# Performance work log

Measured on AMD Instinct MI355X. Metric: run time of the kernel, lower is better.

The kernel has to match this reference:

```python
import jax, jax.numpy as jnp
import numpy as np

GROUP_SIZE = 128
LORA_ALPHA = 32
R = 16
SCALING = LORA_ALPHA / R  # lora_alpha / r


def setup_inputs() -> dict:
    key = jax.random.key(0)
    k1, k2, k3, k4, k5, k6 = jax.random.split(key, 6)
    B, S, IN, OUT = 8, 16, 4096, 11008
    G = IN // GROUP_SIZE  # 32 quantization groups
    x = jax.random.normal(k1, (B, S, IN), dtype=jnp.float32)
    int_weight = jax.random.randint(k2, (IN, OUT), 0, 16, dtype=jnp.int32)  # int4 codes
    zeros = jax.random.randint(k3, (G, OUT), 0, 16, dtype=jnp.int32)        # per-group zero points
    scales = jax.random.uniform(k4, (G, OUT), dtype=jnp.float32) * 0.02     # per-group scales
    lora_A = jax.random.normal(k5, (R, IN), dtype=jnp.float32) * (1.0 / np.sqrt(IN))
    lora_B = jax.random.normal(k6, (OUT, R), dtype=jnp.float32) * 0.02
    return {"x": x, "int_weight": int_weight, "zeros": zeros,
            "scales": scales, "lora_A": lora_A, "lora_B": lora_B}


def reference(x, int_weight, zeros, scales, lora_A, lora_B):
    # Dequantize int4 weights: w[i, o] = (q[i, o] - zero[g(i), o]) * scale[g(i), o]
    zeros_f = jnp.repeat(zeros.astype(jnp.float32), GROUP_SIZE, axis=0)   # [IN, OUT]
    scales_f = jnp.repeat(scales, GROUP_SIZE, axis=0)                     # [IN, OUT]
    w = (int_weight.astype(jnp.float32) - zeros_f) * scales_f             # [IN, OUT]
    # qlinear: x @ W_deq
    base = jnp.einsum('bsi,io->bso', x, w)
    # LoRA: x @ A^T @ B^T * scaling  (dropout=0 -> identity)
    lora = jnp.einsum('bsr,or->bso', jnp.einsum('bsi,ri->bsr', x, lora_A), lora_B)
    return base + lora * SCALING
```

## Files before the change

### kernel.cpp

```cpp
#include <hip/hip_runtime.h>
#include <hip/hip_bf16.h>

typedef __bf16 bf16_t;
typedef __bf16 bf16x8 __attribute__((ext_vector_type(8)));
typedef __bf16 bf16x4 __attribute__((ext_vector_type(4)));
typedef float f32x4 __attribute__((ext_vector_type(4)));

#define M_TOK 128
#define K_IN 4096
#define N_OUT 11008
#define R_LORA 16
#define SCALING 2.0f

__global__ __launch_bounds__(256) void k_prep(const float* __restrict__ x,
                                              const float* __restrict__ loraA,
                                              float* __restrict__ T,
                                              bf16_t* __restrict__ xb) {
  const int m = blockIdx.x;
  __shared__ float xs[K_IN];
  const float4* xr = (const float4*)(x + (size_t)m * K_IN);
  bf16x4* xbr = (bf16x4*)(xb + (size_t)m * K_IN);
  for (int i = threadIdx.x; i < K_IN / 4; i += 256) {
    float4 v = xr[i];
    ((float4*)xs)[i] = v;
    bf16x4 pv = {(bf16_t)v.x, (bf16_t)v.y, (bf16_t)v.z, (bf16_t)v.w};
    xbr[i] = pv;
  }
  __syncthreads();
  const int w = threadIdx.x >> 6;
  const int lane = threadIdx.x & 63;
  float a0 = 0.f, a1 = 0.f, a2 = 0.f, a3 = 0.f;
  const float4* A0 = (const float4*)(loraA + (size_t)(w * 4 + 0) * K_IN);
  const float4* A1 = (const float4*)(loraA + (size_t)(w * 4 + 1) * K_IN);
  const float4* A2 = (const float4*)(loraA + (size_t)(w * 4 + 2) * K_IN);
  const float4* A3 = (const float4*)(loraA + (size_t)(w * 4 + 3) * K_IN);
  for (int i = lane; i < K_IN / 4; i += 64) {
    float4 xv = ((float4*)xs)[i];
    float4 v0 = A0[i], v1 = A1[i], v2 = A2[i], v3 = A3[i];
    a0 += xv.x * v0.x + xv.y * v0.y + xv.z * v0.z + xv.w * v0.w;
    a1 += xv.x * v1.x + xv.y * v1.y + xv.z * v1.z + xv.w * v1.w;
    a2 += xv.x * v2.x + xv.y * v2.y + xv.z * v2.z + xv.w * v2.w;
    a3 += xv.x * v3.x + xv.y * v3.y + xv.z * v3.z + xv.w * v3.w;
  }
#pragma unroll
  for (int off = 32; off; off >>= 1) {
    a0 += __shfl_down(a0, off);
    a1 += __shfl_down(a1, off);
    a2 += __shfl_down(a2, off);
    a3 += __shfl_down(a3, off);
  }
  if (lane == 0) {
    float* tm = T + m * R_LORA + w * 4;
    tm[0] = a0 * SCALING;
    tm[1] = a1 * SCALING;
    tm[2] = a2 * SCALING;
    tm[3] = a3 * SCALING;
  }
}

__global__ __launch_bounds__(256) void k_lora(const float* __restrict__ T,
                                              const float* __restrict__ loraB,
                                              float* __restrict__ out) {
  const int b = blockIdx.x;
  const int m = b / 43;
  const int o = (b % 43) * 256 + threadIdx.x;
  const float* t = T + m * R_LORA;
  const float4* br = (const float4*)(loraB + (size_t)o * R_LORA);
  float4 b0 = br[0], b1 = br[1], b2 = br[2], b3 = br[3];
  float s = t[0] * b0.x + t[1] * b0.y + t[2] * b0.z + t[3] * b0.w +
            t[4] * b1.x + t[5] * b1.y + t[6] * b1.z + t[7] * b1.w +
            t[8] * b2.x + t[9] * b2.y + t[10] * b2.z + t[11] * b2.w +
            t[12] * b3.x + t[13] * b3.y + t[14] * b3.z + t[15] * b3.w;
  out[(size_t)m * N_OUT + o] = s;
}

#define NSTRIPS 172
#define WSTRIDE 72

__global__ __launch_bounds__(256, 4) void k_main(const int* __restrict__ qw,
                                                 const int* __restrict__ zr,
                                                 const float* __restrict__ sc,
                                                 const bf16_t* __restrict__ xb,
                                                 float* __restrict__ out) {
  const int nb = blockIdx.x % NSTRIPS;
  const int kc = blockIdx.x / NSTRIPS;
  const int o0 = nb * 64;
  const int k0 = kc * 1024;

  __shared__ __align__(16) bf16_t wlds[2][64 * WSTRIDE];

  const int tid = threadIdx.x;
  const int w = tid >> 6;
  const int lane = tid & 63;
  const int oq = lane;
  const int kq = w * 16;
  const int ocol = o0 + oq;
  const int* qp = qw + (size_t)(k0 + kq) * N_OUT + ocol;

  float sf[8], nzs[8];
  {
    const int g0 = k0 >> 7;
#pragma unroll
    for (int g = 0; g < 8; ++g) {
      float s_ = sc[(size_t)(g0 + g) * N_OUT + ocol];
      int z_ = zr[(size_t)(g0 + g) * N_OUT + ocol];
      sf[g] = s_;
      nzs[g] = -(float)z_ * s_;
    }
  }

  int qr[16];
#pragma unroll
  for (int j = 0; j < 16; ++j) qr[j] = qp[(size_t)j * N_OUT];
  {
    bf16x8 wv0, wv1;
#pragma unroll
    for (int j = 0; j < 8; ++j) {
      wv0[j] = (bf16_t)fmaf((float)qr[j], sf[0], nzs[0]);
      wv1[j] = (bf16_t)fmaf((float)qr[8 + j], sf[0], nzs[0]);
    }
    *(bf16x8*)&wlds[0][oq * WSTRIDE + kq] = wv0;
    *(bf16x8*)&wlds[0][oq * WSTRIDE + kq + 8] = wv1;
  }

  f32x4 acc[2][4];
#pragma unroll
  for (int mt = 0; mt < 2; ++mt)
#pragma unroll
    for (int ot = 0; ot < 4; ++ot) acc[mt][ot] = (f32x4){0.f, 0.f, 0.f, 0.f};

  const int aq = (lane >> 4) * 8;
  const bf16_t* ap = xb + (size_t)(w * 32 + (lane & 15)) * K_IN + k0 + aq;

#pragma unroll
  for (int step = 0; step < 16; ++step) {
    __syncthreads();
    const int buf = step & 1;

    if (step + 1 < 16) {
      const int* qn = qp + (size_t)(step + 1) * 64 * N_OUT;
#pragma unroll
      for (int j = 0; j < 16; ++j) qr[j] = qn[(size_t)j * N_OUT];
    }

#pragma unroll
    for (int ks = 0; ks < 2; ++ks) {
      bf16x8 a0 = *(const bf16x8*)(ap + step * 64 + ks * 32);
      bf16x8 a1 = *(const bf16x8*)(ap + (size_t)16 * K_IN + step * 64 + ks * 32);
#pragma unroll
      for (int ot = 0; ot < 4; ++ot) {
        bf16x8 bfrag =
            *(bf16x8*)&wlds[buf][(ot * 16 + (lane & 15)) * WSTRIDE + ks * 32 + aq];
        acc[0][ot] = __builtin_amdgcn_mfma_f32_16x16x32_bf16(a0, bfrag, acc[0][ot], 0, 0, 0);
        acc[1][ot] = __builtin_amdgcn_mfma_f32_16x16x32_bf16(a1, bfrag, acc[1][ot], 0, 0, 0);
      }
    }

    if (step + 1 < 16) {
      const int g = (step + 1) >> 1;
      bf16x8 wv0, wv1;
#pragma unroll
      for (int j = 0; j < 8; ++j) {
        wv0[j] = (bf16_t)fmaf((float)qr[j], sf[g], nzs[g]);
        wv1[j] = (bf16_t)fmaf((float)qr[8 + j], sf[g], nzs[g]);
      }
      *(bf16x8*)&wlds[1 - buf][oq * WSTRIDE + kq] = wv0;
      *(bf16x8*)&wlds[1 - buf][oq * WSTRIDE + kq + 8] = wv1;
    }
  }

#pragma unroll
  for (int mt = 0; mt < 2; ++mt) {
    const int m = w * 32 + mt * 16 + ((lane >> 4) << 2);
#pragma unroll
    for (int ot = 0; ot < 4; ++ot) {
      const int o = o0 + ot * 16 + (lane & 15);
#pragma unroll
      for (int r = 0; r < 4; ++r)
        unsafeAtomicAdd(&out[(size_t)(m + r) * N_OUT + o], acc[mt][ot][r]);
    }
  }
}

extern "C" void kernel_launch(void* const* d_in, const int* in_sizes, int n_in,
                              void* d_out, int out_size, void* d_ws, size_t ws_size,
                              hipStream_t stream) {
  const float* x = (const float*)d_in[0];
  const int* qw = (const int*)d_in[1];
  const int* zr = (const int*)d_in[2];
  const float* sc = (const float*)d_in[3];
  const float* loraA = (const float*)d_in[4];
  const float* loraB = (const float*)d_in[5];
  float* out = (float*)d_out;

  float* T = (float*)d_ws;
  bf16_t* xb = (bf16_t*)((char*)d_ws + 8192);

  k_prep<<<dim3(M_TOK), dim3(256), 0, stream>>>(x, loraA, T, xb);
  k_lora<<<dim3(M_TOK * 43), dim3(256), 0, stream>>>(T, loraB, out);
  k_main<<<dim3(NSTRIPS * 4), dim3(256), 0, stream>>>(qw, zr, sc, xb, out);
}
```

Baseline: 292.7 us.

## Restructure main GEMM into 16-column tiles with in-block split-K reduction and fused LoRA epilogue

The main kernel now gives each block a 16-wide output strip covering all 128 tokens. Its four waves each take a quarter of K, dequantize weights straight into registers as MFMA B fragments with no LDS staging, and reduce through shared memory. The LoRA B projection is fused into the epilogue, so the separate k_lora kernel and the global atomics go away and outputs are written with plain vector stores. The prep kernel writes x in an MFMA-fragment-friendly bf16 layout so A loads are coalesced. The cost is that A fragments are re-read from global/L2 by every block, and occupancy hint drops to 3.

```diff
diff --git a/kernel.cpp b/kernel.cpp
--- a/kernel.cpp
+++ b/kernel.cpp
@@ -3,7 +3,6 @@
 
 typedef __bf16 bf16_t;
 typedef __bf16 bf16x8 __attribute__((ext_vector_type(8)));
-typedef __bf16 bf16x4 __attribute__((ext_vector_type(4)));
 typedef float f32x4 __attribute__((ext_vector_type(4)));
 
 #define M_TOK 128
@@ -11,20 +10,28 @@
 #define N_OUT 11008
 #define R_LORA 16
 #define SCALING 2.0f
+#define NTILE 688
 
 __global__ __launch_bounds__(256) void k_prep(const float* __restrict__ x,
                                               const float* __restrict__ loraA,
                                               float* __restrict__ T,
-                                              bf16_t* __restrict__ xb) {
+                                              bf16_t* __restrict__ xf) {
   const int m = blockIdx.x;
+  const int mt = m >> 4;
+  const int ml = m & 15;
   __shared__ float xs[K_IN];
   const float4* xr = (const float4*)(x + (size_t)m * K_IN);
-  bf16x4* xbr = (bf16x4*)(xb + (size_t)m * K_IN);
-  for (int i = threadIdx.x; i < K_IN / 4; i += 256) {
-    float4 v = xr[i];
-    ((float4*)xs)[i] = v;
-    bf16x4 pv = {(bf16_t)v.x, (bf16_t)v.y, (bf16_t)v.z, (bf16_t)v.w};
-    xbr[i] = pv;
+#pragma unroll
+  for (int c0 = 0; c0 < 2; ++c0) {
+    const int c = c0 * 256 + threadIdx.x;
+    float4 vA = xr[2 * c], vB = xr[2 * c + 1];
+    ((float4*)xs)[2 * c] = vA;
+    ((float4*)xs)[2 * c + 1] = vB;
+    bf16x8 pv = {(bf16_t)vA.x, (bf16_t)vA.y, (bf16_t)vA.z, (bf16_t)vA.w,
+                 (bf16_t)vB.x, (bf16_t)vB.y, (bf16_t)vB.z, (bf16_t)vB.w};
+    const int ks = c >> 2;
+    const int lq = (c & 3) * 16 + ml;
+    *(bf16x8*)(xf + ((size_t)(mt * 128 + ks) * 64 + lq) * 8) = pv;
   }
   __syncthreads();
   const int w = threadIdx.x >> 6;
@@ -58,44 +65,27 @@
   }
 }
 
-__global__ __launch_bounds__(256) void k_lora(const float* __restrict__ T,
-                                              const float* __restrict__ loraB,
-                                              float* __restrict__ out) {
-  const int b = blockIdx.x;
-  const int m = b / 43;
-  const int o = (b % 43) * 256 + threadIdx.x;
-  const float* t = T + m * R_LORA;
-  const float4* br = (const float4*)(loraB + (size_t)o * R_LORA);
-  float4 b0 = br[0], b1 = br[1], b2 = br[2], b3 = br[3];
-  float s = t[0] * b0.x + t[1] * b0.y + t[2] * b0.z + t[3] * b0.w +
-            t[4] * b1.x + t[5] * b1.y + t[6] * b1.z + t[7] * b1.w +
-            t[8] * b2.x + t[9] * b2.y + t[10] * b2.z + t[11] * b2.w +
-            t[12] * b3.x + t[13] * b3.y + t[14] * b3.z + t[15] * b3.w;
-  out[(size_t)m * N_OUT + o] = s;
-}
-
-#define NSTRIPS 172
-#define WSTRIDE 72
-
-__global__ __launch_bounds__(256, 4) void k_main(const int* __restrict__ qw,
+__global__ __launch_bounds__(256, 3) void k_main(const int* __restrict__ qw,
                                                  const int* __restrict__ zr,
                                                  const float* __restrict__ sc,
-                                                 const bf16_t* __restrict__ xb,
+                                                 const bf16_t* __restrict__ xf,
+                                                 const float* __restrict__ T,
+                                                 const float* __restrict__ loraB,
                                                  float* __restrict__ out) {
-  const int nb = blockIdx.x % NSTRIPS;
-  const int kc = blockIdx.x / NSTRIPS;
-  const int o0 = nb * 64;
-  const int k0 = kc * 1024;
-
-  __shared__ __align__(16) bf16_t wlds[2][64 * WSTRIDE];
-
+  const int nt = (blockIdx.x & 7) * 86 + (blockIdx.x >> 3);
+  const int o0 = nt * 16;
   const int tid = threadIdx.x;
   const int w = tid >> 6;
   const int lane = tid & 63;
-  const int oq = lane;
-  const int kq = w * 16;
-  const int ocol = o0 + oq;
-  const int* qp = qw + (size_t)(k0 + kq) * N_OUT + ocol;
+  const int ol = lane & 15;
+  const int ocol = o0 + ol;
+  const int krow = (lane >> 4) * 8;
+  const int k0 = w * 1024;
+
+  __shared__ float red[4][M_TOK * 16];
+  __shared__ float lb[256];
+
+  lb[tid] = loraB[(size_t)o0 * R_LORA + tid];
 
   float sf[8], nzs[8];
   {
@@ -109,77 +99,88 @@
     }
   }
 
-  int qr[16];
-#pragma unroll
-  for (int j = 0; j < 16; ++j) qr[j] = qp[(size_t)j * N_OUT];
+  const int* qp = qw + (size_t)(k0 + krow) * N_OUT + ocol;
+  const bf16_t* ap = xf + ((size_t)(k0 >> 5) * 64 + lane) * 8;
+
+  int qA[8], qB[8];
+#pragma unroll
+  for (int j = 0; j < 8; ++j) qA[j] = qp[(size_t)j * N_OUT];
   {
-    bf16x8 wv0, wv1;
-#pragma unroll
-    for (int j = 0; j < 8; ++j) {
-      wv0[j] = (bf16_t)fmaf((float)qr[j], sf[0], nzs[0]);
-      wv1[j] = (bf16_t)fmaf((float)qr[8 + j], sf[0], nzs[0]);
-    }
-    *(bf16x8*)&wlds[0][oq * WSTRIDE + kq] = wv0;
-    *(bf16x8*)&wlds[0][oq * WSTRIDE + kq + 8] = wv1;
-  }
-
-  f32x4 acc[2][4];
-#pragma unroll
-  for (int mt = 0; mt < 2; ++mt)
-#pragma unroll
-    for (int ot = 0; ot < 4; ++ot) acc[mt][ot] = (f32x4){0.f, 0.f, 0.f, 0.f};
-
-  const int aq = (lane >> 4) * 8;
-  const bf16_t* ap = xb + (size_t)(w * 32 + (lane & 15)) * K_IN + k0 + aq;
-
-#pragma unroll
-  for (int step = 0; step < 16; ++step) {
-    __syncthreads();
-    const int buf = step & 1;
-
-    if (step + 1 < 16) {
-      const int* qn = qp + (size_t)(step + 1) * 64 * N_OUT;
-#pragma unroll
-      for (int j = 0; j < 16; ++j) qr[j] = qn[(size_t)j * N_OUT];
-    }
-
-#pragma unroll
-    for (int ks = 0; ks < 2; ++ks) {
-      bf16x8 a0 = *(const bf16x8*)(ap + step * 64 + ks * 32);
-      bf16x8 a1 = *(const bf16x8*)(ap + (size_t)16 * K_IN + step * 64 + ks * 32);
-#pragma unroll
-      for (int ot = 0; ot < 4; ++ot) {
-        bf16x8 bfrag =
-            *(bf16x8*)&wlds[buf][(ot * 16 + (lane & 15)) * WSTRIDE + ks * 32 + aq];
-        acc[0][ot] = __builtin_amdgcn_mfma_f32_16x16x32_bf16(a0, bfrag, acc[0][ot], 0, 0, 0);
-        acc[1][ot] = __builtin_amdgcn_mfma_f32_16x16x32_bf16(a1, bfrag, acc[1][ot], 0, 0, 0);
-      }
-    }
-
-    if (step + 1 < 16) {
-      const int g = (step + 1) >> 1;
-      bf16x8 wv0, wv1;
-#pragma unroll
-      for (int j = 0; j < 8; ++j) {
-        wv0[j] = (bf16_t)fmaf((float)qr[j], sf[g], nzs[g]);
-        wv1[j] = (bf16_t)fmaf((float)qr[8 + j], sf[g], nzs[g]);
-      }
-      *(bf16x8*)&wlds[1 - buf][oq * WSTRIDE + kq] = wv0;
-      *(bf16x8*)&wlds[1 - buf][oq * WSTRIDE + kq + 8] = wv1;
-    }
-  }
-
-#pragma unroll
-  for (int mt = 0; mt < 2; ++mt) {
-    const int m = w * 32 + mt * 16 + ((lane >> 4) << 2);
-#pragma unroll
-    for (int ot = 0; ot < 4; ++ot) {
-      const int o = o0 + ot * 16 + (lane & 15);
-#pragma unroll
-      for (int r = 0; r < 4; ++r)
-        unsafeAtomicAdd(&out[(size_t)(m + r) * N_OUT + o], acc[mt][ot][r]);
-    }
-  }
+    const int* qn = qp + (size_t)32 * N_OUT;
+#pragma unroll
+    for (int j = 0; j < 8; ++j) qB[j] = qn[(size_t)j * N_OUT];
+  }
+
+  f32x4 acc[8];
+#pragma unroll
+  for (int mt = 0; mt < 8; ++mt) acc[mt] = (f32x4){0.f, 0.f, 0.f, 0.f};
+
+  for (int kk = 0; kk < 32; kk += 2) {
+    const int g = kk >> 2;
+    bf16x8 bfA;
+#pragma unroll
+    for (int j = 0; j < 8; ++j) bfA[j] = (bf16_t)fmaf((float)qA[j], sf[g], nzs[g]);
+    if (kk < 30) {
+      const int* qn = qp + (size_t)(kk + 2) * 32 * N_OUT;
+#pragma unroll
+      for (int j = 0; j < 8; ++j) qA[j] = qn[(size_t)j * N_OUT];
+    }
+#pragma unroll
+    for (int mt = 0; mt < 8; ++mt) {
+      bf16x8 a = *(const bf16x8*)(ap + ((size_t)mt * 128 + kk) * 512);
+      acc[mt] = __builtin_amdgcn_mfma_f32_16x16x32_bf16(a, bfA, acc[mt], 0, 0, 0);
+    }
+    bf16x8 bfB;
+#pragma unroll
+    for (int j = 0; j < 8; ++j) bfB[j] = (bf16_t)fmaf((float)qB[j], sf[g], nzs[g]);
+    if (kk < 30) {
+      const int* qn = qp + (size_t)(kk + 3) * 32 * N_OUT;
+#pragma unroll
+      for (int j = 0; j < 8; ++j) qB[j] = qn[(size_t)j * N_OUT];
+    }
+#pragma unroll
+    for (int mt = 0; mt < 8; ++mt) {
+      bf16x8 a = *(const bf16x8*)(ap + ((size_t)mt * 128 + kk + 1) * 512);
+      acc[mt] = __builtin_amdgcn_mfma_f32_16x16x32_bf16(a, bfB, acc[mt], 0, 0, 0);
+    }
+  }
+
+#pragma unroll
+  for (int mt = 0; mt < 8; ++mt) {
+    const int mbase = mt * 16 + ((lane >> 4) << 2);
+#pragma unroll
+    for (int r = 0; r < 4; ++r) red[w][(mbase + r) * 16 + ol] = acc[mt][r];
+  }
+  __syncthreads();
+
+  const int m = tid >> 1;
+  const int ob = (tid & 1) * 8;
+  float tr[16];
+  {
+    const float4* Tm4 = (const float4*)(T + (size_t)m * R_LORA);
+#pragma unroll
+    for (int q = 0; q < 4; ++q) {
+      float4 tv = Tm4[q];
+      tr[q * 4 + 0] = tv.x;
+      tr[q * 4 + 1] = tv.y;
+      tr[q * 4 + 2] = tv.z;
+      tr[q * 4 + 3] = tv.w;
+    }
+  }
+  float res[8];
+#pragma unroll
+  for (int i = 0; i < 8; ++i) {
+    const int e = m * 16 + ob + i;
+    float s = red[0][e] + red[1][e] + red[2][e] + red[3][e];
+    const float* lr = &lb[(ob + i) * R_LORA];
+    float tv = 0.f;
+#pragma unroll
+    for (int r = 0; r < 16; ++r) tv = fmaf(tr[r], lr[r], tv);
+    res[i] = s + tv;
+  }
+  float4* op = (float4*)(out + (size_t)m * N_OUT + o0 + ob);
+  op[0] = (float4){res[0], res[1], res[2], res[3]};
+  op[1] = (float4){res[4], res[5], res[6], res[7]};
 }
 
 extern "C" void kernel_launch(void* const* d_in, const int* in_sizes, int n_in,
@@ -194,9 +195,8 @@
   float* out = (float*)d_out;
 
   float* T = (float*)d_ws;
-  bf16_t* xb = (bf16_t*)((char*)d_ws + 8192);
-
-  k_prep<<<dim3(M_TOK), dim3(256), 0, stream>>>(x, loraA, T, xb);
-  k_lora<<<dim3(M_TOK * 43), dim3(256), 0, stream>>>(T, loraB, out);
-  k_main<<<dim3(NSTRIPS * 4), dim3(256), 0, stream>>>(qw, zr, sc, xb, out);
+  bf16_t* xf = (bf16_t*)((char*)d_ws + 8192);
+
+  k_prep<<<dim3(M_TOK), dim3(256), 0, stream>>>(x, loraA, T, xf);
+  k_main<<<dim3(NTILE), dim3(256), 0, stream>>>(qw, zr, sc, xf, T, loraB, out);
 }
```

New measurement: 319.8 us. 9.2% more time.

## Deepen weight prefetch to two stages and pre-swizzle bf16 activations into MFMA fragments

Applied to the files above, without the earlier changes.

The main loop now keeps two register sets of int4 codes in flight, issuing global loads two steps ahead instead of one, so more latency of the weight stream is hidden behind the MFMAs. The prep kernel also writes x in a fragment-major layout so each lane's A-operand load is one contiguous 16-byte read with lanes adjacent, rather than strided row accesses. The cost is 16 more live registers per thread, which may pressure the 4-blocks-per-SIMD occupancy target.

```diff
diff --git a/kernel.cpp b/kernel.cpp
--- a/kernel.cpp
+++ b/kernel.cpp
@@ -3,7 +3,6 @@
 
 typedef __bf16 bf16_t;
 typedef __bf16 bf16x8 __attribute__((ext_vector_type(8)));
-typedef __bf16 bf16x4 __attribute__((ext_vector_type(4)));
 typedef float f32x4 __attribute__((ext_vector_type(4)));
 
 #define M_TOK 128
@@ -11,20 +10,29 @@
 #define N_OUT 11008
 #define R_LORA 16
 #define SCALING 2.0f
+#define NSTRIPS 172
+#define WSTRIDE 72
 
 __global__ __launch_bounds__(256) void k_prep(const float* __restrict__ x,
                                               const float* __restrict__ loraA,
                                               float* __restrict__ T,
-                                              bf16_t* __restrict__ xb) {
+                                              bf16_t* __restrict__ xf) {
   const int m = blockIdx.x;
+  const int mt = m >> 4;
+  const int ml = m & 15;
   __shared__ float xs[K_IN];
   const float4* xr = (const float4*)(x + (size_t)m * K_IN);
-  bf16x4* xbr = (bf16x4*)(xb + (size_t)m * K_IN);
-  for (int i = threadIdx.x; i < K_IN / 4; i += 256) {
-    float4 v = xr[i];
-    ((float4*)xs)[i] = v;
-    bf16x4 pv = {(bf16_t)v.x, (bf16_t)v.y, (bf16_t)v.z, (bf16_t)v.w};
-    xbr[i] = pv;
+#pragma unroll
+  for (int c0 = 0; c0 < 2; ++c0) {
+    const int c = c0 * 256 + threadIdx.x;
+    float4 vA = xr[2 * c], vB = xr[2 * c + 1];
+    ((float4*)xs)[2 * c] = vA;
+    ((float4*)xs)[2 * c + 1] = vB;
+    bf16x8 pv = {(bf16_t)vA.x, (bf16_t)vA.y, (bf16_t)vA.z, (bf16_t)vA.w,
+                 (bf16_t)vB.x, (bf16_t)vB.y, (bf16_t)vB.z, (bf16_t)vB.w};
+    const int ks = c >> 2;
+    const int lq = (c & 3) * 16 + ml;
+    *(bf16x8*)(xf + ((size_t)(mt * 128 + ks) * 64 + lq) * 8) = pv;
   }
   __syncthreads();
   const int w = threadIdx.x >> 6;
@@ -74,13 +82,10 @@
   out[(size_t)m * N_OUT + o] = s;
 }
 
-#define NSTRIPS 172
-#define WSTRIDE 72
-
 __global__ __launch_bounds__(256, 4) void k_main(const int* __restrict__ qw,
                                                  const int* __restrict__ zr,
                                                  const float* __restrict__ sc,
-                                                 const bf16_t* __restrict__ xb,
+                                                 const bf16_t* __restrict__ xf,
                                                  float* __restrict__ out) {
   const int nb = blockIdx.x % NSTRIPS;
   const int kc = blockIdx.x / NSTRIPS;
@@ -109,15 +114,17 @@
     }
   }
 
-  int qr[16];
-#pragma unroll
-  for (int j = 0; j < 16; ++j) qr[j] = qp[(size_t)j * N_OUT];
+  int qrA[16], qrB[16];
+#pragma unroll
+  for (int j = 0; j < 16; ++j) qrA[j] = qp[(size_t)j * N_OUT];
+#pragma unroll
+  for (int j = 0; j < 16; ++j) qrB[j] = qp[(size_t)(64 + j) * N_OUT];
   {
     bf16x8 wv0, wv1;
 #pragma unroll
     for (int j = 0; j < 8; ++j) {
-      wv0[j] = (bf16_t)fmaf((float)qr[j], sf[0], nzs[0]);
-      wv1[j] = (bf16_t)fmaf((float)qr[8 + j], sf[0], nzs[0]);
+      wv0[j] = (bf16_t)fmaf((float)qrA[j], sf[0], nzs[0]);
+      wv1[j] = (bf16_t)fmaf((float)qrA[8 + j], sf[0], nzs[0]);
     }
     *(bf16x8*)&wlds[0][oq * WSTRIDE + kq] = wv0;
     *(bf16x8*)&wlds[0][oq * WSTRIDE + kq + 8] = wv1;
@@ -129,44 +136,54 @@
 #pragma unroll
     for (int ot = 0; ot < 4; ++ot) acc[mt][ot] = (f32x4){0.f, 0.f, 0.f, 0.f};
 
+  const bf16_t* ap = xf + (size_t)lane * 8;
   const int aq = (lane >> 4) * 8;
-  const bf16_t* ap = xb + (size_t)(w * 32 + (lane & 15)) * K_IN + k0 + aq;
-
-#pragma unroll
-  for (int step = 0; step < 16; ++step) {
+  const int ol = lane & 15;
+
+#define MFMA_STEP(STEP, BUF)                                                       \
+  {                                                                                \
+    _Pragma("unroll") for (int ks = 0; ks < 2; ++ks) {                             \
+      const int ksg = kc * 32 + (STEP)*2 + ks;                                     \
+      bf16x8 a0 = *(const bf16x8*)(ap + ((size_t)((2 * w) * 128 + ksg)) * 512);    \
+      bf16x8 a1 = *(const bf16x8*)(ap + ((size_t)((2 * w + 1) * 128 + ksg)) * 512);\
+      _Pragma("unroll") for (int ot = 0; ot < 4; ++ot) {                           \
+        bf16x8 bfrag = *(bf16x8*)&wlds[BUF][(ot * 16 + ol) * WSTRIDE + ks * 32 + aq];\
+        acc[0][ot] = __builtin_amdgcn_mfma_f32_16x16x32_bf16(a0, bfrag, acc[0][ot], 0, 0, 0); \
+        acc[1][ot] = __builtin_amdgcn_mfma_f32_16x16x32_bf16(a1, bfrag, acc[1][ot], 0, 0, 0); \
+      }                                                                            \
+    }                                                                              \
+  }
+
+#define DEQ_STORE(QR, G, BUF)                                                      \
+  {                                                                                \
+    bf16x8 wv0, wv1;                                                               \
+    _Pragma("unroll") for (int j = 0; j < 8; ++j) {                                \
+      wv0[j] = (bf16_t)fmaf((float)QR[j], sf[G], nzs[G]);                          \
+      wv1[j] = (bf16_t)fmaf((float)QR[8 + j], sf[G], nzs[G]);                      \
+    }                                                                              \
+    *(bf16x8*)&wlds[BUF][oq * WSTRIDE + kq] = wv0;                                 \
+    *(bf16x8*)&wlds[BUF][oq * WSTRIDE + kq + 8] = wv1;                             \
+  }
+
+#pragma unroll
+  for (int s2 = 0; s2 < 8; ++s2) {
+    const int step = s2 * 2;
     __syncthreads();
-    const int buf = step & 1;
-
-    if (step + 1 < 16) {
-      const int* qn = qp + (size_t)(step + 1) * 64 * N_OUT;
-#pragma unroll
-      for (int j = 0; j < 16; ++j) qr[j] = qn[(size_t)j * N_OUT];
-    }
-
-#pragma unroll
-    for (int ks = 0; ks < 2; ++ks) {
-      bf16x8 a0 = *(const bf16x8*)(ap + step * 64 + ks * 32);
-      bf16x8 a1 = *(const bf16x8*)(ap + (size_t)16 * K_IN + step * 64 + ks * 32);
-#pragma unroll
-      for (int ot = 0; ot < 4; ++ot) {
-        bf16x8 bfrag =
-            *(bf16x8*)&wlds[buf][(ot * 16 + (lane & 15)) * WSTRIDE + ks * 32 + aq];
-        acc[0][ot] = __builtin_amdgcn_mfma_f32_16x16x32_bf16(a0, bfrag, acc[0][ot], 0, 0, 0);
-        acc[1][ot] = __builtin_amdgcn_mfma_f32_16x16x32_bf16(a1, bfrag, acc[1][ot], 0, 0, 0);
-      }
-    }
-
-    if (step + 1 < 16) {
-      const int g = (step + 1) >> 1;
-      bf16x8 wv0, wv1;
-#pragma unroll
-      for (int j = 0; j < 8; ++j) {
-        wv0[j] = (bf16_t)fmaf((float)qr[j], sf[g], nzs[g]);
-        wv1[j] = (bf16_t)fmaf((float)qr[8 + j], sf[g], nzs[g]);
-      }
-      *(bf16x8*)&wlds[1 - buf][oq * WSTRIDE + kq] = wv0;
-      *(bf16x8*)&wlds[1 - buf][oq * WSTRIDE + kq + 8] = wv1;
-    }
+    if (step + 2 < 16) {
+      const int* qn = qp + (size_t)(step + 2) * 64 * N_OUT;
+#pragma unroll
+      for (int j = 0; j < 16; ++j) qrA[j] = qn[(size_t)j * N_OUT];
+    }
+    MFMA_STEP(step, 0)
+    DEQ_STORE(qrB, (step + 1) >> 1, 1)
+    __syncthreads();
+    if (step + 3 < 16) {
+      const int* qn = qp + (size_t)(step + 3) * 64 * N_OUT;
+#pragma unroll
+      for (int j = 0; j < 16; ++j) qrB[j] = qn[(size_t)j * N_OUT];
+    }
+    MFMA_STEP(step + 1, 1)
+    if (step + 2 < 16) DEQ_STORE(qrA, (step + 2) >> 1, 0)
   }
 
 #pragma unroll
@@ -174,12 +191,14 @@
     const int m = w * 32 + mt * 16 + ((lane >> 4) << 2);
 #pragma unroll
     for (int ot = 0; ot < 4; ++ot) {
-      const int o = o0 + ot * 16 + (lane & 15);
+      const int o = o0 + ot * 16 + ol;
 #pragma unroll
       for (int r = 0; r < 4; ++r)
         unsafeAtomicAdd(&out[(size_t)(m + r) * N_OUT + o], acc[mt][ot][r]);
     }
   }
+#undef MFMA_STEP
+#undef DEQ_STORE
 }
 
 extern "C" void kernel_launch(void* const* d_in, const int* in_sizes, int n_in,
@@ -194,9 +213,9 @@
   float* out = (float*)d_out;
 
   float* T = (float*)d_ws;
-  bf16_t* xb = (bf16_t*)((char*)d_ws + 8192);
-
-  k_prep<<<dim3(M_TOK), dim3(256), 0, stream>>>(x, loraA, T, xb);
+  bf16_t* xf = (bf16_t*)((char*)d_ws + 8192);
+
+  k_prep<<<dim3(M_TOK), dim3(256), 0, stream>>>(x, loraA, T, xf);
   k_lora<<<dim3(M_TOK * 43), dim3(256), 0, stream>>>(T, loraB, out);
-  k_main<<<dim3(NSTRIPS * 4), dim3(256), 0, stream>>>(qw, zr, sc, xb, out);
-}
+  k_main<<<dim3(NSTRIPS * 4), dim3(256), 0, stream>>>(qw, zr, sc, xf, out);
+}
```

Result: no change. 290.7 us (-0.7%).
